# Optimization experiments

Measured on AMD Instinct MI355X. Metric: run time of the kernel, lower is better.

## Reference

```python
import jax, jax.numpy as jnp
import numpy as np

N, C, CW, H, W = 8, 128, 64, 96, 96
NUM_BASES, KS = 6, 3
TEM = 6  # len(bases) for ks=3 (one scale, 6 FB bases)


def _conv2d(x, w, b, pad):
    y = jax.lax.conv_general_dilated(
        x, w, window_strides=(1, 1), padding=[(pad, pad), (pad, pad)],
        dimension_numbers=("NCHW", "OIHW", "NCHW"))
    return y + b[None, :, None, None]


def setup_inputs() -> dict:
    key = jax.random.key(0)
    ks = jax.random.split(key, 9)
    feat = jax.random.normal(ks[0], (N, C, H, W), jnp.float32)
    weight = jax.random.normal(ks[1], (N, CW, H, W), jnp.float32)
    # conv_bases: Conv2d(C+CW -> C, 3x3) -> tanh -> Conv2d(C -> NUM_BASES*TEM, 1x1) -> tanh
    fan1 = (C + CW) * 9
    conv1_w = jax.random.normal(ks[2], (C, C + CW, 3, 3), jnp.float32) / np.sqrt(fan1)
    conv1_b = jnp.zeros((C,), jnp.float32)
    conv2_w = jax.random.normal(ks[3], (NUM_BASES * TEM, C, 1, 1), jnp.float32) / np.sqrt(C)
    conv2_b = jnp.zeros((NUM_BASES * TEM,), jnp.float32)
    # fixed FB bases buffer, shape (TEM, KS*KS); stand-in normalized random basis
    bb = jax.random.normal(ks[4], (TEM, KS * KS), jnp.float32)
    bases_buf = bb / jnp.linalg.norm(bb, axis=1, keepdims=True)
    # coef: (C, C*NUM_BASES, 1, 1), kaiming fan_out
    coef = jax.random.normal(ks[5], (C, C * NUM_BASES, 1, 1), jnp.float32) * np.sqrt(2.0 / C)
    bias = jnp.zeros((C,), jnp.float32)
    return {"feat": feat, "weight": weight, "conv1_w": conv1_w, "conv1_b": conv1_b,
            "conv2_w": conv2_w, "conv2_b": conv2_b, "bases_buf": bases_buf,
            "coef": coef, "bias": bias}


def reference(feat, weight, conv1_w, conv1_b, conv2_w, conv2_b, bases_buf, coef, bias):
    n, c, h, w = feat.shape
    x = jnp.concatenate([feat, weight], axis=1)
    hmid = jnp.tanh(_conv2d(x, conv1_w, conv1_b, 1))
    b = jnp.tanh(_conv2d(hmid, conv2_w, conv2_b, 0))  # (N, NUM_BASES*TEM, H, W)
    b = b.reshape(n, NUM_BASES, TEM, h, w)
    # combine learned coefficients with fixed FB bases -> per-pixel filters
    bases = jnp.einsum("bmkhw,kl->bmlhw", b, bases_buf)  # (N, M, KS*KS, H, W)
    # im2col (torch F.unfold ordering: channel-major, kernel row-major)
    padded = jnp.pad(feat, ((0, 0), (0, 0), (1, 1), (1, 1)))
    patches = jnp.stack([padded[:, :, i:i + h, j:j + w]
                         for i in range(KS) for j in range(KS)], axis=2)  # (N,C,9,H,W)
    bases_out = jnp.einsum("bmlhw,bclhw->bcmhw", bases, patches)
    bases_out = bases_out.reshape(n, c * NUM_BASES, h, w)
    # 1x1 conv with coef + bias
    out = jnp.einsum("bkhw,ck->bchw", bases_out, coef[:, :, 0, 0]) + bias[None, :, None, None]
    return out
```

## Files before the change

### kernel.cpp

```cpp
#include <hip/hip_runtime.h>

#define NN   8
#define CC   128
#define CWW  64
#define CIN  192
#define HH   96
#define WW_  96
#define HW   (HH*WW_)
#define NB   6
#define TEM  6
#define B36  36
#define KF   768

typedef __attribute__((ext_vector_type(8))) short bf16x8;
typedef __attribute__((ext_vector_type(4))) float f32x4;

#define OFF_A1     0
#define OFF_A2     110592
#define OFF_BASES  159744
#define OFF_HMID   4141056

__device__ inline ushort f2bf(float f) {
    union { float f; unsigned u; } x; x.f = f;
    unsigned r = x.u + 0x7FFFu + ((x.u >> 16) & 1u);
    return (ushort)(r >> 16);
}
__device__ inline float bf2f(ushort h) {
    union { unsigned u; float f; } t; t.u = ((unsigned)h) << 16; return t.f;
}
__device__ inline float fast_tanh(float x) {
    x = fminf(fmaxf(x, -15.f), 15.f);
    float e = __expf(2.f * x);
    float r;
    asm volatile("v_rcp_f32 %0, %1" : "=v"(r) : "v"(e + 1.f));
    return (e - 1.f) * r;
}

__global__ __launch_bounds__(256) void k_prep(const float* __restrict__ w1,
                                              const float* __restrict__ coef,
                                              ushort* __restrict__ A1,
                                              ushort* __restrict__ A2) {
    int i = blockIdx.x * 256 + threadIdx.x;
    if (i < 221184) {
        int j = i & 7, l = (i >> 3) & 63, mf = (i >> 9) & 7, ks = i >> 12;
        int kc = ks / 9, tap = ks - kc * 9;
        int co = mf * 16 + (l & 15);
        int ci = kc * 32 + 8 * (l >> 4) + j;
        A1[i] = f2bf(w1[(co * CIN + ci) * 9 + tap]);
    } else {
        int t = i - 221184;
        if (t < 98304) {
            int j = t & 7, l = (t >> 3) & 63, cf = (t >> 9) & 7, r = t >> 12;
            int ks = r & 3, m = r >> 2;
            int co = cf * 16 + (l & 15);
            int ci = ks * 32 + 8 * (l >> 4) + j;
            A2[t] = f2bf(coef[co * KF + ci * 6 + m]);
        }
    }
}

#define SBS 40
__global__ __launch_bounds__(256, 2) void k_conv1m(const float* __restrict__ feat,
                                                   const float* __restrict__ wgt,
                                                   const ushort* __restrict__ A1,
                                                   const float* __restrict__ b1,
                                                   ushort* __restrict__ hmid) {
    const int w0 = blockIdx.x * 16, h0 = blockIdx.y * 16, n = blockIdx.z;
    __shared__ ushort sB[2][324 * SBS];
    __shared__ ushort sA[2][4096];
    const int tid = threadIdx.x;
    const int l = tid & 63, wv = tid >> 6, lx = l & 15, cg = l >> 4;

    f32x4 acc[8][4];
    const f32x4 z = {0.f, 0.f, 0.f, 0.f};
#pragma unroll
    for (int mf = 0; mf < 8; ++mf)
#pragma unroll
        for (int nf = 0; nf < 4; ++nf) acc[mf][nf] = z;

#pragma unroll 1
    for (int it = 0; it < 21; ++it) {
        int i = it * 256 + tid;
        if (i < 5184) {
            int cpair = i / 324, col = i - cpair * 324;
            int rp = col / 18, xl = col - rp * 18;
            int gh = h0 - 1 + rp, gw = w0 - 1 + xl;
            int cp = cpair * 2;
            unsigned v = 0u;
            if ((unsigned)gh < 96u && (unsigned)gw < 96u) {
                const float* fp = &feat[((size_t)(n * CC + cp)) * HW + gh * WW_ + gw];
                v = (unsigned)f2bf(fp[0]) | ((unsigned)f2bf(fp[HW]) << 16);
            }
            *(unsigned*)&sB[0][col * SBS + cp] = v;
        }
    }
    {
        const uint4* src = (const uint4*)A1;
        uint4 v0 = src[tid], v1 = src[256 + tid];
        ((uint4*)&sA[0][0])[tid] = v0;
        ((uint4*)&sA[0][0])[256 + tid] = v1;
    }
    __syncthreads();

#pragma unroll 1
    for (int kc = 0; kc < 6; ++kc) {
#pragma unroll 1
        for (int tap = 0; tap < 9; ++tap) {
            const int ks = kc * 9 + tap;
            const int ab = ks & 1, bb = kc & 1;

            uint4 pA0, pA1;
            const bool doA = (ks < 53);
            if (doA) {
                const uint4* src = (const uint4*)(A1 + (size_t)(ks + 1) * 4096);
                pA0 = src[tid]; pA1 = src[256 + tid];
            }

            float pB0a = 0.f, pB0b = 0.f, pB1a = 0.f, pB1b = 0.f, pB2a = 0.f, pB2b = 0.f;
            int bo0 = -1, bo1 = -1, bo2 = -1;
            const bool doB = (kc < 5) && (tap < 7);
            if (doB) {
                const int nkc = kc + 1;
#pragma unroll
                for (int it = 0; it < 3; ++it) {
                    int i = (tap * 3 + it) * 256 + tid;
                    if (i < 5184) {
                        int cpair = i / 324, col = i - cpair * 324;
                        int rp = col / 18, xl = col - rp * 18;
                        int gh = h0 - 1 + rp, gw = w0 - 1 + xl;
                        int cp = cpair * 2, ci = nkc * 32 + cp;
                        float va = 0.f, vb = 0.f;
                        if ((unsigned)gh < 96u && (unsigned)gw < 96u) {
                            const float* fp = (ci < CC)
                                ? &feat[((size_t)(n * CC + ci)) * HW + gh * WW_ + gw]
                                : &wgt[((size_t)(n * CWW + ci - CC)) * HW + gh * WW_ + gw];
                            va = fp[0]; vb = fp[HW];
                        }
                        int off = col * SBS + cp;
                        if (it == 0)      { pB0a = va; pB0b = vb; bo0 = off; }
                        else if (it == 1) { pB1a = va; pB1b = vb; bo1 = off; }
                        else              { pB2a = va; pB2b = vb; bo2 = off; }
                    }
                }
            }

            bf16x8 afr[8];
#pragma unroll
            for (int mf = 0; mf < 8; ++mf)
                afr[mf] = *(const bf16x8*)&sA[ab][(mf * 64 + l) * 8];
            const int dy = tap / 3, dx = tap - dy * 3;
            bf16x8 bfr[4];
#pragma unroll
            for (int nf = 0; nf < 4; ++nf) {
                int col0 = (wv * 4 + nf + dy) * 18 + lx + dx;
                bfr[nf] = *(const bf16x8*)&sB[bb][col0 * SBS + 8 * cg];
            }
#pragma unroll
            for (int mf = 0; mf < 8; ++mf)
#pragma unroll
                for (int nf = 0; nf < 4; ++nf)
                    acc[mf][nf] = __builtin_amdgcn_mfma_f32_16x16x32_bf16(afr[mf], bfr[nf], acc[mf][nf], 0, 0, 0);

            if (doA) {
                uint4* d = (uint4*)&sA[ab ^ 1][0];
                d[tid] = pA0; d[256 + tid] = pA1;
            }
            if (doB) {
                ushort* nb = &sB[bb ^ 1][0];
                if (bo0 >= 0) *(unsigned*)&nb[bo0] = (unsigned)f2bf(pB0a) | ((unsigned)f2bf(pB0b) << 16);
                if (bo1 >= 0) *(unsigned*)&nb[bo1] = (unsigned)f2bf(pB1a) | ((unsigned)f2bf(pB1b) << 16);
                if (bo2 >= 0) *(unsigned*)&nb[bo2] = (unsigned)f2bf(pB2a) | ((unsigned)f2bf(pB2b) << 16);
            }
            __syncthreads();
        }
    }

#pragma unroll
    for (int mf = 0; mf < 8; ++mf)
#pragma unroll
        for (int nf = 0; nf < 4; ++nf) {
            const int h = h0 + wv * 4 + nf;
#pragma unroll
            for (int r = 0; r < 4; ++r) {
                int co = mf * 16 + cg * 4 + r;
                float x = acc[mf][nf][r] + b1[co];
                hmid[((size_t)(n * CC + co) * HH + h) * WW_ + w0 + lx] = f2bf(fast_tanh(x));
            }
        }
}

__global__ __launch_bounds__(256) void k_conv2(const ushort* __restrict__ hmid,
                                               const float* __restrict__ w2,
                                               const float* __restrict__ b2,
                                               const float* __restrict__ bbuf,
                                               float* __restrict__ bases) {
    __shared__ float sW2[B36 * CC];
    __shared__ float sBB[TEM * 9];
    for (int i = threadIdx.x; i < B36 * CC; i += 256) sW2[i] = w2[i];
    if (threadIdx.x < TEM * 9) sBB[threadIdx.x] = bbuf[threadIdx.x];
    __syncthreads();

    const int n   = blockIdx.y;
    const int pix = blockIdx.x * 256 + threadIdx.x;

    float a[B36];
#pragma unroll
    for (int k = 0; k < B36; ++k) a[k] = b2[k];

    const ushort* hp = &hmid[(size_t)(n * CC) * HW + pix];
    for (int c = 0; c < CC; ++c) {
        float hv = bf2f(hp[c * HW]);
#pragma unroll
        for (int k = 0; k < B36; ++k) a[k] = fmaf(hv, sW2[k * CC + c], a[k]);
    }
#pragma unroll
    for (int k = 0; k < B36; ++k) a[k] = fast_tanh(a[k]);

    float* bp = &bases[(size_t)(n * 54) * HW + pix];
#pragma unroll
    for (int m = 0; m < NB; ++m) {
#pragma unroll
        for (int ll = 0; ll < 9; ++ll) {
            float s = 0.f;
#pragma unroll
            for (int t = 0; t < TEM; ++t) s = fmaf(a[m * TEM + t], sBB[t * 9 + ll], s);
            bp[(m * 9 + ll) * HW] = s;
        }
    }
}

#define FMT 134
__global__ __launch_bounds__(512) void k_fused(const float* __restrict__ feat,
                                               const ushort* __restrict__ A2,
                                               const float* __restrict__ bases,
                                               const float* __restrict__ bias,
                                               float* __restrict__ out) {
    const int wt = blockIdx.x, ht = blockIdx.y, n = blockIdx.z;
    const int w0 = wt * 32, h0 = ht * 3;
    __shared__ ushort sFeat[176 * 128];
    __shared__ ushort sFm[176 * FMT];
    __shared__ float  sBa[54 * 96];
    const int tid = threadIdx.x;

    for (int it = 0; it < 22; ++it) {
        int i = it * 512 + tid;
        if (i < 170 * 64) {
            int hp = i % 170;
            int cp = (i / 170) * 2;
            int hy2 = hp / 34, hx2 = hp - hy2 * 34;
            int gh = h0 - 1 + hy2, gw = w0 - 1 + hx2;
            unsigned v = 0u;
            if ((unsigned)gh < 96u && (unsigned)gw < 96u) {
                const float* fp = &feat[((size_t)(n * CC + cp)) * HW + gh * WW_ + gw];
                v = (unsigned)f2bf(fp[0]) | ((unsigned)f2bf(fp[HW]) << 16);
            }
            int idx = hp * 128 + (((cp >> 3) ^ (hp & 15)) << 3) + (cp & 7);
            *(unsigned*)&sFeat[idx] = v;
        }
    }
    for (int j = tid; j < 6 * 64; j += 512) ((unsigned*)&sFeat[170 * 128])[j] = 0u;
    for (int it = 0; it < 11; ++it) {
        int i = it * 512 + tid;
        if (i < 54 * 96) {
            int j = i / 96, p = i - j * 96;
            int hy = p >> 5, wx = p & 31;
            sBa[i] = bases[((size_t)(n * 54 + j)) * HW + (h0 + hy) * WW_ + w0 + wx];
        }
    }
    __syncthreads();

    const int l  = tid & 63, wv = tid >> 6;
    const int lx = l & 15, cg = l >> 4;
    const int mg = wv & 1, ng = wv >> 1;
    const int nt = (ng == 3) ? 2 : 3;
    const int co_l = tid & 127;
    const int g4   = tid >> 7;
    const int wx0  = g4 * 8;

    float accO[3][8];
#pragma unroll
    for (int a = 0; a < 3; ++a)
#pragma unroll
        for (int p = 0; p < 8; ++p) accO[a][p] = 0.f;

    const bf16x8* Ap = (const bf16x8*)A2;
    const f32x4 z = {0.f, 0.f, 0.f, 0.f};

    for (int m = 0; m < 6; ++m) {
        __syncthreads();

        f32x4 acc[4][3];
#pragma unroll
        for (int mi = 0; mi < 4; ++mi)
#pragma unroll
            for (int ti = 0; ti < 3; ++ti) acc[mi][ti] = z;

#pragma unroll
        for (int ks = 0; ks < 4; ++ks) {
            bf16x8 a[4];
#pragma unroll
            for (int mi = 0; mi < 4; ++mi)
                a[mi] = Ap[((size_t)((m * 4 + ks) * 8 + mg * 4 + mi)) * 64 + l];
            const int gsw = (ks * 4 + cg) ^ lx;
#pragma unroll
            for (int ti = 0; ti < 3; ++ti) {
                if (ti < nt) {
                    int px = (ng * 3 + ti) * 16 + lx;
                    bf16x8 b = *(const bf16x8*)&sFeat[px * 128 + (gsw << 3)];
#pragma unroll
                    for (int mi = 0; mi < 4; ++mi)
                        acc[mi][ti] = __builtin_amdgcn_mfma_f32_16x16x32_bf16(a[mi], b, acc[mi][ti], 0, 0, 0);
                }
            }
        }
#pragma unroll
        for (int ti = 0; ti < 3; ++ti) {
            if (ti < nt) {
                int px = (ng * 3 + ti) * 16 + lx;
#pragma unroll
                for (int mi = 0; mi < 4; ++mi) {
                    int co = (mg * 4 + mi) * 16 + cg * 4;
                    unsigned v0 = (unsigned)f2bf(acc[mi][ti][0]) | ((unsigned)f2bf(acc[mi][ti][1]) << 16);
                    unsigned v1 = (unsigned)f2bf(acc[mi][ti][2]) | ((unsigned)f2bf(acc[mi][ti][3]) << 16);
                    *(unsigned*)&sFm[px * FMT + co]     = v0;
                    *(unsigned*)&sFm[px * FMT + co + 2] = v1;
                }
            }
        }
        __syncthreads();

#pragma unroll
        for (int hy = 0; hy < 3; ++hy) {
#pragma unroll
            for (int dy = 0; dy < 3; ++dy) {
                const int hrow = (hy + dy) * 34 + wx0;
                float rr[10];
#pragma unroll
                for (int x = 0; x < 10; ++x)
                    rr[x] = bf2f(sFm[(hrow + x) * FMT + co_l]);
#pragma unroll
                for (int dx = 0; dx < 3; ++dx) {
                    const float* sb = &sBa[(m * 9 + dy * 3 + dx) * 96 + hy * 32 + wx0];
#pragma unroll
                    for (int p = 0; p < 8; ++p)
                        accO[hy][p] = fmaf(sb[p], rr[p + dx], accO[hy][p]);
                }
            }
        }
    }

    const float bv = bias[co_l];
#pragma unroll
    for (int hy = 0; hy < 3; ++hy) {
        float4 o0, o1;
        o0.x = accO[hy][0] + bv; o0.y = accO[hy][1] + bv;
        o0.z = accO[hy][2] + bv; o0.w = accO[hy][3] + bv;
        o1.x = accO[hy][4] + bv; o1.y = accO[hy][5] + bv;
        o1.z = accO[hy][6] + bv; o1.w = accO[hy][7] + bv;
        float* op = &out[((size_t)(n * CC + co_l)) * HW + (h0 + hy) * WW_ + w0 + wx0];
        *(float4*)op       = o0;
        *(float4*)(op + 4) = o1;
    }
}

extern "C" void kernel_launch(void* const* d_in, const int* in_sizes, int n_in,
                              void* d_out, int out_size, void* d_ws, size_t ws_size,
                              hipStream_t stream) {
    const float* feat = (const float*)d_in[0];
    const float* wgt  = (const float*)d_in[1];
    const float* w1   = (const float*)d_in[2];
    const float* b1   = (const float*)d_in[3];
    const float* w2   = (const float*)d_in[4];
    const float* b2   = (const float*)d_in[5];
    const float* bbuf = (const float*)d_in[6];
    const float* coef = (const float*)d_in[7];
    const float* bias = (const float*)d_in[8];
    float* out = (float*)d_out;

    float* ws = (float*)d_ws;
    ushort* A1   = (ushort*)(ws + OFF_A1);
    ushort* A2   = (ushort*)(ws + OFF_A2);
    float* bases = ws + OFF_BASES;
    ushort* hmid = (ushort*)(ws + OFF_HMID);

    k_prep  <<<dim3(1248),      dim3(256), 0, stream>>>(w1, coef, A1, A2);
    k_conv1m<<<dim3(6, 6, NN),  dim3(256), 0, stream>>>(feat, wgt, A1, b1, hmid);
    k_conv2 <<<dim3(36, NN),    dim3(256), 0, stream>>>(hmid, w2, b2, bbuf, bases);
    k_fused <<<dim3(3, 32, NN), dim3(512), 0, stream>>>(feat, A2, bases, bias, out);
}
```

Before: 361.0 us.

## Shrink fused tile to 16 wide with 256 threads, store bases as bf16

The fused kernel now uses 16x3 output tiles with 256-thread blocks and launch bounds allowing two blocks per CU, which doubles the grid and shrinks shared memory per block. The epilogue is restructured so each thread handles two adjacent channels over 4 pixels, reading each feature-map row once and reusing it across output rows. The per-pixel bases buffer is written and read as bf16 to halve that intermediate's traffic. Smaller tiles recompute more halo in the MFMA stage (90 of 96 pixel slots versus 170 of 176), and bf16 bases lose some precision.

```diff
diff --git a/kernel.cpp b/kernel.cpp
--- a/kernel.cpp
+++ b/kernel.cpp
@@ -193,7 +193,7 @@
                                                const float* __restrict__ w2,
                                                const float* __restrict__ b2,
                                                const float* __restrict__ bbuf,
-                                               float* __restrict__ bases) {
+                                               ushort* __restrict__ bases) {
     __shared__ float sW2[B36 * CC];
     __shared__ float sBB[TEM * 9];
     for (int i = threadIdx.x; i < B36 * CC; i += 256) sW2[i] = w2[i];
@@ -216,7 +216,7 @@
 #pragma unroll
     for (int k = 0; k < B36; ++k) a[k] = fast_tanh(a[k]);
 
-    float* bp = &bases[(size_t)(n * 54) * HW + pix];
+    ushort* bp = &bases[(size_t)(n * 54) * HW + pix];
 #pragma unroll
     for (int m = 0; m < NB; ++m) {
 #pragma unroll
@@ -224,30 +224,32 @@
             float s = 0.f;
 #pragma unroll
             for (int t = 0; t < TEM; ++t) s = fmaf(a[m * TEM + t], sBB[t * 9 + ll], s);
-            bp[(m * 9 + ll) * HW] = s;
-        }
-    }
-}
-
-#define FMT 134
-__global__ __launch_bounds__(512) void k_fused(const float* __restrict__ feat,
-                                               const ushort* __restrict__ A2,
-                                               const float* __restrict__ bases,
-                                               const float* __restrict__ bias,
-                                               float* __restrict__ out) {
+            bp[(m * 9 + ll) * HW] = f2bf(s);
+        }
+    }
+}
+
+#define FMT2 130
+__global__ __launch_bounds__(256, 2) void k_fused(const float* __restrict__ feat,
+                                                  const ushort* __restrict__ A2,
+                                                  const ushort* __restrict__ bases,
+                                                  const float* __restrict__ bias,
+                                                  float* __restrict__ out) {
     const int wt = blockIdx.x, ht = blockIdx.y, n = blockIdx.z;
-    const int w0 = wt * 32, h0 = ht * 3;
-    __shared__ ushort sFeat[176 * 128];
-    __shared__ ushort sFm[176 * FMT];
-    __shared__ float  sBa[54 * 96];
+    const int w0 = wt * 16, h0 = ht * 3;
+    __shared__ ushort sFeat[96 * 128];
+    __shared__ ushort sFm[96 * FMT2];
+    __shared__ float  sBa[54 * 48];
     const int tid = threadIdx.x;
 
-    for (int it = 0; it < 22; ++it) {
-        int i = it * 512 + tid;
-        if (i < 170 * 64) {
-            int hp = i % 170;
-            int cp = (i / 170) * 2;
-            int hy2 = hp / 34, hx2 = hp - hy2 * 34;
+#pragma unroll 1
+    for (int it = 0; it < 23; ++it) {
+        int i = it * 256 + tid;
+        if (i < 5760) {
+            int cp2 = i / 90;
+            int hp  = i - cp2 * 90;
+            int cp  = cp2 * 2;
+            int hy2 = hp / 18, hx2 = hp - hy2 * 18;
             int gh = h0 - 1 + hy2, gw = w0 - 1 + hx2;
             unsigned v = 0u;
             if ((unsigned)gh < 96u && (unsigned)gw < 96u) {
@@ -258,13 +260,18 @@
             *(unsigned*)&sFeat[idx] = v;
         }
     }
-    for (int j = tid; j < 6 * 64; j += 512) ((unsigned*)&sFeat[170 * 128])[j] = 0u;
+#pragma unroll
+    for (int it = 0; it < 2; ++it) {
+        int i = it * 256 + tid;
+        if (i < 384) ((unsigned*)&sFeat[90 * 128])[i] = 0u;
+    }
+#pragma unroll 1
     for (int it = 0; it < 11; ++it) {
-        int i = it * 512 + tid;
-        if (i < 54 * 96) {
-            int j = i / 96, p = i - j * 96;
-            int hy = p >> 5, wx = p & 31;
-            sBa[i] = bases[((size_t)(n * 54 + j)) * HW + (h0 + hy) * WW_ + w0 + wx];
+        int i = it * 256 + tid;
+        if (i < 54 * 48) {
+            int j = i / 48, p = i - j * 48;
+            int hy = p >> 4, wx = p & 15;
+            sBa[i] = bf2f(bases[((size_t)(n * 54 + j)) * HW + (h0 + hy) * WW_ + w0 + wx]);
         }
     }
     __syncthreads();
@@ -272,20 +279,21 @@
     const int l  = tid & 63, wv = tid >> 6;
     const int lx = l & 15, cg = l >> 4;
     const int mg = wv & 1, ng = wv >> 1;
-    const int nt = (ng == 3) ? 2 : 3;
-    const int co_l = tid & 127;
-    const int g4   = tid >> 7;
-    const int wx0  = g4 * 8;
-
-    float accO[3][8];
-#pragma unroll
-    for (int a = 0; a < 3; ++a)
-#pragma unroll
-        for (int p = 0; p < 8; ++p) accO[a][p] = 0.f;
+    const int cp = tid & 63;
+    const int g4 = tid >> 6;
+
+    float accO[3][2][4];
+#pragma unroll
+    for (int hy = 0; hy < 3; ++hy)
+#pragma unroll
+        for (int j = 0; j < 2; ++j)
+#pragma unroll
+            for (int p = 0; p < 4; ++p) accO[hy][j][p] = 0.f;
 
     const bf16x8* Ap = (const bf16x8*)A2;
     const f32x4 z = {0.f, 0.f, 0.f, 0.f};
 
+#pragma unroll 1
     for (int m = 0; m < 6; ++m) {
         __syncthreads();
 
@@ -301,66 +309,70 @@
 #pragma unroll
             for (int mi = 0; mi < 4; ++mi)
                 a[mi] = Ap[((size_t)((m * 4 + ks) * 8 + mg * 4 + mi)) * 64 + l];
-            const int gsw = (ks * 4 + cg) ^ lx;
+            const int gsw = ((ks * 4 + cg) ^ lx) << 3;
 #pragma unroll
             for (int ti = 0; ti < 3; ++ti) {
-                if (ti < nt) {
-                    int px = (ng * 3 + ti) * 16 + lx;
-                    bf16x8 b = *(const bf16x8*)&sFeat[px * 128 + (gsw << 3)];
-#pragma unroll
-                    for (int mi = 0; mi < 4; ++mi)
-                        acc[mi][ti] = __builtin_amdgcn_mfma_f32_16x16x32_bf16(a[mi], b, acc[mi][ti], 0, 0, 0);
+                int px = (ng * 3 + ti) * 16 + lx;
+                bf16x8 b = *(const bf16x8*)&sFeat[px * 128 + gsw];
+#pragma unroll
+                for (int mi = 0; mi < 4; ++mi)
+                    acc[mi][ti] = __builtin_amdgcn_mfma_f32_16x16x32_bf16(a[mi], b, acc[mi][ti], 0, 0, 0);
+            }
+        }
+#pragma unroll
+        for (int ti = 0; ti < 3; ++ti) {
+            int px = (ng * 3 + ti) * 16 + lx;
+#pragma unroll
+            for (int mi = 0; mi < 4; ++mi) {
+                int co = (mg * 4 + mi) * 16 + cg * 4;
+                unsigned v0 = (unsigned)f2bf(acc[mi][ti][0]) | ((unsigned)f2bf(acc[mi][ti][1]) << 16);
+                unsigned v1 = (unsigned)f2bf(acc[mi][ti][2]) | ((unsigned)f2bf(acc[mi][ti][3]) << 16);
+                *(unsigned*)&sFm[px * FMT2 + co]     = v0;
+                *(unsigned*)&sFm[px * FMT2 + co + 2] = v1;
+            }
+        }
+        __syncthreads();
+
+#pragma unroll
+        for (int r = 0; r < 5; ++r) {
+            float rowv[6][2];
+#pragma unroll
+            for (int x = 0; x < 6; ++x) {
+                int hp = r * 18 + g4 * 4 + x;
+                unsigned u = *(const unsigned*)&sFm[hp * FMT2 + cp * 2];
+                rowv[x][0] = bf2f((ushort)(u & 0xffffu));
+                rowv[x][1] = bf2f((ushort)(u >> 16));
+            }
+#pragma unroll
+            for (int hy = 0; hy < 3; ++hy) {
+                const int dy = r - hy;
+                if (dy < 0 || dy > 2) continue;
+#pragma unroll
+                for (int dx = 0; dx < 3; ++dx) {
+                    const float* sb = &sBa[(m * 9 + dy * 3 + dx) * 48 + hy * 16 + g4 * 4];
+#pragma unroll
+                    for (int p = 0; p < 4; ++p) {
+                        float bv = sb[p];
+                        accO[hy][0][p] = fmaf(bv, rowv[p + dx][0], accO[hy][0][p]);
+                        accO[hy][1][p] = fmaf(bv, rowv[p + dx][1], accO[hy][1][p]);
+                    }
                 }
             }
         }
-#pragma unroll
-        for (int ti = 0; ti < 3; ++ti) {
-            if (ti < nt) {
-                int px = (ng * 3 + ti) * 16 + lx;
-#pragma unroll
-                for (int mi = 0; mi < 4; ++mi) {
-                    int co = (mg * 4 + mi) * 16 + cg * 4;
-                    unsigned v0 = (unsigned)f2bf(acc[mi][ti][0]) | ((unsigned)f2bf(acc[mi][ti][1]) << 16);
-                    unsigned v1 = (unsigned)f2bf(acc[mi][ti][2]) | ((unsigned)f2bf(acc[mi][ti][3]) << 16);
-                    *(unsigned*)&sFm[px * FMT + co]     = v0;
-                    *(unsigned*)&sFm[px * FMT + co + 2] = v1;
-                }
-            }
-        }
-        __syncthreads();
-
-#pragma unroll
-        for (int hy = 0; hy < 3; ++hy) {
-#pragma unroll
-            for (int dy = 0; dy < 3; ++dy) {
-                const int hrow = (hy + dy) * 34 + wx0;
-                float rr[10];
-#pragma unroll
-                for (int x = 0; x < 10; ++x)
-                    rr[x] = bf2f(sFm[(hrow + x) * FMT + co_l]);
-#pragma unroll
-                for (int dx = 0; dx < 3; ++dx) {
-                    const float* sb = &sBa[(m * 9 + dy * 3 + dx) * 96 + hy * 32 + wx0];
-#pragma unroll
-                    for (int p = 0; p < 8; ++p)
-                        accO[hy][p] = fmaf(sb[p], rr[p + dx], accO[hy][p]);
-                }
-            }
-        }
-    }
-
-    const float bv = bias[co_l];
-#pragma unroll
-    for (int hy = 0; hy < 3; ++hy) {
-        float4 o0, o1;
-        o0.x = accO[hy][0] + bv; o0.y = accO[hy][1] + bv;
-        o0.z = accO[hy][2] + bv; o0.w = accO[hy][3] + bv;
-        o1.x = accO[hy][4] + bv; o1.y = accO[hy][5] + bv;
-        o1.z = accO[hy][6] + bv; o1.w = accO[hy][7] + bv;
-        float* op = &out[((size_t)(n * CC + co_l)) * HW + (h0 + hy) * WW_ + w0 + wx0];
-        *(float4*)op       = o0;
-        *(float4*)(op + 4) = o1;
-    }
+    }
+
+    const float bv0 = bias[2 * cp], bv1 = bias[2 * cp + 1];
+#pragma unroll
+    for (int hy = 0; hy < 3; ++hy)
+#pragma unroll
+        for (int j = 0; j < 2; ++j) {
+            const int co = 2 * cp + j;
+            const float bb = j ? bv1 : bv0;
+            float4 o;
+            o.x = accO[hy][j][0] + bb; o.y = accO[hy][j][1] + bb;
+            o.z = accO[hy][j][2] + bb; o.w = accO[hy][j][3] + bb;
+            *(float4*)&out[((size_t)(n * CC + co)) * HW + (h0 + hy) * WW_ + w0 + g4 * 4] = o;
+        }
 }
 
 extern "C" void kernel_launch(void* const* d_in, const int* in_sizes, int n_in,
@@ -378,13 +390,13 @@
     float* out = (float*)d_out;
 
     float* ws = (float*)d_ws;
-    ushort* A1   = (ushort*)(ws + OFF_A1);
-    ushort* A2   = (ushort*)(ws + OFF_A2);
-    float* bases = ws + OFF_BASES;
-    ushort* hmid = (ushort*)(ws + OFF_HMID);
+    ushort* A1    = (ushort*)(ws + OFF_A1);
+    ushort* A2    = (ushort*)(ws + OFF_A2);
+    ushort* bases = (ushort*)(ws + OFF_BASES);
+    ushort* hmid  = (ushort*)(ws + OFF_HMID);
 
     k_prep  <<<dim3(1248),      dim3(256), 0, stream>>>(w1, coef, A1, A2);
     k_conv1m<<<dim3(6, 6, NN),  dim3(256), 0, stream>>>(feat, wgt, A1, b1, hmid);
     k_conv2 <<<dim3(36, NN),    dim3(256), 0, stream>>>(hmid, w2, b2, bbuf, bases);
-    k_fused <<<dim3(3, 32, NN), dim3(512), 0, stream>>>(feat, A2, bases, bias, out);
-}
+    k_fused <<<dim3(6, 32, NN), dim3(256), 0, stream>>>(feat, A2, bases, bias, out);
+}
```

New measurement: 334.1 us. 1.08x faster.
